# Kernel optimization log

Measured on AMD Instinct MI355X. Metric: run time of the kernel, lower is better.

The kernel has to match this reference:

```python
import jax, jax.numpy as jnp
import numpy as np

NHID = 1024
NHEAD = 16
HEAD_DIM = 64
B, L = 8, 4096

def setup_inputs() -> dict:
    key = jax.random.key(0)
    ks = jax.random.split(key, 12)
    s_in = 1.0 / np.sqrt(NHID)
    s_o = 1.0 / np.sqrt(NHEAD * HEAD_DIM)
    return {
        'x': jax.random.normal(ks[0], (B, L, NHID), dtype=jnp.float32),
        'ax': jax.random.normal(ks[1], (B, NHID), dtype=jnp.float32),
        'WQ_w': jax.random.normal(ks[2], (NHID, NHEAD * HEAD_DIM), dtype=jnp.float32) * s_in,
        'WQ_b': jnp.zeros((NHEAD * HEAD_DIM,), dtype=jnp.float32),
        'WK_w': jax.random.normal(ks[3], (NHID, NHEAD * HEAD_DIM), dtype=jnp.float32) * s_in,
        'WK_b': jnp.zeros((NHEAD * HEAD_DIM,), dtype=jnp.float32),
        'WV_w': jax.random.normal(ks[4], (NHID, NHEAD * HEAD_DIM), dtype=jnp.float32) * s_in,
        'WV_b': jnp.zeros((NHEAD * HEAD_DIM,), dtype=jnp.float32),
        'WO_w': jax.random.normal(ks[5], (NHEAD * HEAD_DIM, NHID), dtype=jnp.float32) * s_o,
        'WO_b': jnp.zeros((NHID,), dtype=jnp.float32),
    }

def reference(x, ax, WQ_w, WQ_b, WK_w, WK_b, WV_w, WV_b, WO_w, WO_b):
    Bx, Lx, H = x.shape
    nh, d = NHEAD, HEAD_DIM
    q = (x @ WQ_w + WQ_b).reshape(Bx, Lx, nh, d)
    k = (x @ WK_w + WK_b).reshape(Bx, Lx, nh, d)
    # global token projections (note: source's v local slots use K due to pad_v=F.pad(k,...) bug)
    ak = (ax @ WK_w + WK_b).reshape(Bx, 1, nh, d)
    av = (ax @ WV_w + WV_b).reshape(Bx, 1, nh, d)
    # shifted local window (unfold_size=3), pad seq dim by 1 on each side
    pad_k = jnp.pad(k, ((0, 0), (1, 1), (0, 0), (0, 0)))  # (B, L+2, nh, d)
    k_shift = jnp.stack([pad_k[:, t:Lx + t] for t in range(3)], axis=3)  # (B,L,nh,3,d)
    akb = jnp.broadcast_to(ak, (Bx, Lx, nh, d))[:, :, :, None, :]  # (B,L,nh,1,d)
    avb = jnp.broadcast_to(av, (Bx, Lx, nh, d))[:, :, :, None, :]
    K = jnp.concatenate([akb, k_shift], axis=3)  # (B,L,nh,4,d)
    V = jnp.concatenate([avb, k_shift], axis=3)  # local V slots = K (faithful to source bug)
    scores = jnp.einsum('blhd,blhjd->blhj', q, K) / jnp.sqrt(jnp.float32(d))
    alphas = jax.nn.softmax(scores, axis=-1)  # dropout = identity (eval)
    att = jnp.einsum('blhj,blhjd->blhd', alphas, V).reshape(Bx, Lx, nh * d)
    return att @ WO_w + WO_b
```

## Files before the change

### kernel.cpp

```cpp
#include <hip/hip_runtime.h>
#include <hip/hip_bf16.h>

typedef __bf16 bf16x8 __attribute__((ext_vector_type(8)));
typedef __bf16 bf16x4 __attribute__((ext_vector_type(4)));
typedef float  floatx4 __attribute__((ext_vector_type(4)));

#define L_SEQ 4096

__global__ void cvt_bf16_kernel(const float* __restrict__ src,
                                __bf16* __restrict__ dst, int n8)
{
    int i = blockIdx.x * blockDim.x + threadIdx.x;
    if (i >= n8) return;
    const float4* s = (const float4*)src + (size_t)i * 2;
    float4 f0 = s[0], f1 = s[1];
    bf16x8 o;
    o[0] = (__bf16)f0.x; o[1] = (__bf16)f0.y; o[2] = (__bf16)f0.z; o[3] = (__bf16)f0.w;
    o[4] = (__bf16)f1.x; o[5] = (__bf16)f1.y; o[6] = (__bf16)f1.z; o[7] = (__bf16)f1.w;
    *((bf16x8*)dst + i) = o;
}

__global__ void transpose_cvt_kernel(const float* __restrict__ src,
                                     __bf16* __restrict__ dst, int K, int N)
{
    __shared__ float tile[32][33];
    int tx = threadIdx.x & 31, ty = threadIdx.x >> 5;
    int n0 = blockIdx.x * 32, k0 = blockIdx.y * 32;
    #pragma unroll
    for (int i = 0; i < 32; i += 8)
        tile[ty + i][tx] = src[(size_t)(k0 + ty + i) * N + n0 + tx];
    __syncthreads();
    #pragma unroll
    for (int i = 0; i < 32; i += 8)
        dst[(size_t)(n0 + ty + i) * K + k0 + tx] = (__bf16)tile[tx][ty + i];
}

__global__ void akv_kernel(const float* __restrict__ ax,
                           const float* __restrict__ Wk, const float* __restrict__ bk,
                           const float* __restrict__ Wv, const float* __restrict__ bv,
                           float* __restrict__ akv)
{
    int b = blockIdx.x, nb = blockIdx.y, kv = blockIdx.z;
    int n = nb * 256 + threadIdx.x;
    const float* W    = kv ? Wv : Wk;
    const float* bias = kv ? bv : bk;
    const float* axr  = ax + (size_t)b * 1024;
    float acc = bias[n];
    for (int k = 0; k < 1024; ++k)
        acc = fmaf(axr[k], W[(size_t)k * 1024 + n], acc);
    akv[((size_t)b * 2 + kv) * 1024 + n] = acc;
}

template <bool OUT_F32>
__global__ __launch_bounds__(256, 2) void gemm_bt_kernel(
    const __bf16* __restrict__ A, const __bf16* __restrict__ Bt,
    const float* __restrict__ b0, const float* __restrict__ b1, int nsplit,
    void* __restrict__ Cp, int M, int N, int K)
{
    __shared__ __bf16 As[128 * 32];
    __shared__ __bf16 Bs[128 * 32];
    const int tid  = threadIdx.x;
    const int wave = tid >> 6, lane = tid & 63;
    const int quad = lane >> 4, l16 = lane & 15;
    const int m0 = blockIdx.x * 128, n0 = blockIdx.y * 128;
    const int wm = (wave >> 1) * 64, wn = (wave & 1) * 64;

    floatx4 acc[4][4] = {};

    const int srow  = lane >> 2;
    const int skcol = (lane & 3) * 8;

    for (int k0 = 0; k0 < K; k0 += 32) {
        if (k0) __syncthreads();
        #pragma unroll
        for (int c = 0; c < 2; ++c) {
            int chunk = wave * 2 + c;
            int row   = chunk * 16 + srow;
            __builtin_amdgcn_global_load_lds(
                (const __attribute__((address_space(1))) void*)(A + (size_t)(m0 + row) * K + k0 + skcol),
                (__attribute__((address_space(3))) void*)(As + chunk * 512),
                16, 0, 0);
            __builtin_amdgcn_global_load_lds(
                (const __attribute__((address_space(1))) void*)(Bt + (size_t)(n0 + row) * K + k0 + skcol),
                (__attribute__((address_space(3))) void*)(Bs + chunk * 512),
                16, 0, 0);
        }
        __syncthreads();

        bf16x8 af[4], bfr[4];
        #pragma unroll
        for (int mi = 0; mi < 4; ++mi)
            af[mi] = *(const bf16x8*)(As + (wm + mi * 16 + l16) * 32 + quad * 8);
        #pragma unroll
        for (int ni = 0; ni < 4; ++ni)
            bfr[ni] = *(const bf16x8*)(Bs + (wn + ni * 16 + l16) * 32 + quad * 8);
        #pragma unroll
        for (int mi = 0; mi < 4; ++mi)
            #pragma unroll
            for (int ni = 0; ni < 4; ++ni)
                acc[mi][ni] = __builtin_amdgcn_mfma_f32_16x16x32_bf16(
                    af[mi], bfr[ni], acc[mi][ni], 0, 0, 0);
    }

    #pragma unroll
    for (int ni = 0; ni < 4; ++ni) {
        int gn = n0 + wn + ni * 16 + l16;
        float bv = (gn < nsplit) ? b0[gn] : b1[gn - nsplit];
        #pragma unroll
        for (int mi = 0; mi < 4; ++mi) {
            int gm = m0 + wm + mi * 16 + quad * 4;
            #pragma unroll
            for (int r = 0; r < 4; ++r) {
                float v = acc[mi][ni][r] + bv;
                if (OUT_F32)
                    ((float*)Cp)[(size_t)(gm + r) * N + gn] = v;
                else
                    ((__bf16*)Cp)[(size_t)(gm + r) * N + gn] = (__bf16)v;
            }
        }
    }
}

__global__ void attn_kernel(const __bf16* __restrict__ qk,
                            const float* __restrict__ akv,
                            __bf16* __restrict__ att)
{
    const int m = blockIdx.x;
    const int l = m & (L_SEQ - 1);
    const int b = m >> 12;
    const int t = threadIdx.x;
    const int c4 = t * 4;

    bf16x4 qv = *(const bf16x4*)(qk + (size_t)m * 2048 + c4);
    float q0 = qv[0], q1 = qv[1], q2 = qv[2], q3 = qv[3];

    float kx[3][4];
    #pragma unroll
    for (int j = 0; j < 3; ++j) {
        int ll = l + j - 1;
        if (ll >= 0 && ll < L_SEQ) {
            bf16x4 kv = *(const bf16x4*)(qk + (size_t)(m + j - 1) * 2048 + 1024 + c4);
            kx[j][0] = kv[0]; kx[j][1] = kv[1]; kx[j][2] = kv[2]; kx[j][3] = kv[3];
        } else {
            kx[j][0] = kx[j][1] = kx[j][2] = kx[j][3] = 0.f;
        }
    }
    const float* akp = akv + ((size_t)b * 2 + 0) * 1024 + c4;
    const float* avp = akv + ((size_t)b * 2 + 1) * 1024 + c4;
    float a0 = akp[0], a1 = akp[1], a2 = akp[2], a3 = akp[3];
    float v0 = avp[0], v1 = avp[1], v2 = avp[2], v3 = avp[3];

    float p0 = q0 * a0 + q1 * a1 + q2 * a2 + q3 * a3;
    float p1 = q0 * kx[0][0] + q1 * kx[0][1] + q2 * kx[0][2] + q3 * kx[0][3];
    float p2 = q0 * kx[1][0] + q1 * kx[1][1] + q2 * kx[1][2] + q3 * kx[1][3];
    float p3 = q0 * kx[2][0] + q1 * kx[2][1] + q2 * kx[2][2] + q3 * kx[2][3];
    #pragma unroll
    for (int off = 1; off < 16; off <<= 1) {
        p0 += __shfl_xor(p0, off, 64);
        p1 += __shfl_xor(p1, off, 64);
        p2 += __shfl_xor(p2, off, 64);
        p3 += __shfl_xor(p3, off, 64);
    }
    const float sc = 0.125f;
    float s0 = p0 * sc, s1 = p1 * sc, s2 = p2 * sc, s3 = p3 * sc;
    float mx = fmaxf(fmaxf(s0, s1), fmaxf(s2, s3));
    float e0 = __expf(s0 - mx), e1 = __expf(s1 - mx), e2 = __expf(s2 - mx), e3 = __expf(s3 - mx);
    float inv = 1.f / (e0 + e1 + e2 + e3);

    bf16x4 o;
    o[0] = (__bf16)((e0 * v0 + e1 * kx[0][0] + e2 * kx[1][0] + e3 * kx[2][0]) * inv);
    o[1] = (__bf16)((e0 * v1 + e1 * kx[0][1] + e2 * kx[1][1] + e3 * kx[2][1]) * inv);
    o[2] = (__bf16)((e0 * v2 + e1 * kx[0][2] + e2 * kx[1][2] + e3 * kx[2][2]) * inv);
    o[3] = (__bf16)((e0 * v3 + e1 * kx[0][3] + e2 * kx[1][3] + e3 * kx[2][3]) * inv);
    *(bf16x4*)(att + (size_t)m * 1024 + c4) = o;
}

extern "C" void kernel_launch(void* const* d_in, const int* in_sizes, int n_in,
                              void* d_out, int out_size, void* d_ws, size_t ws_size,
                              hipStream_t stream)
{
    const float* x    = (const float*)d_in[0];
    const float* ax   = (const float*)d_in[1];
    const float* WQ_w = (const float*)d_in[2];
    const float* WQ_b = (const float*)d_in[3];
    const float* WK_w = (const float*)d_in[4];
    const float* WK_b = (const float*)d_in[5];
    const float* WV_w = (const float*)d_in[6];
    const float* WV_b = (const float*)d_in[7];
    const float* WO_w = (const float*)d_in[8];
    const float* WO_b = (const float*)d_in[9];
    float* out = (float*)d_out;

    const int M = 8 * 4096;

    char* ws = (char*)d_ws;
    __bf16* xb   = (__bf16*)(ws);
    __bf16* Wqk  = (__bf16*)(ws + 67108864);
    __bf16* Wo   = (__bf16*)(ws + 71303168);
    __bf16* qk   = (__bf16*)(ws + 73400320);
    __bf16* att  = (__bf16*)(ws + 207618048);
    float*  akv  = (float*)(ws + 274726912);

    {
        int n8 = (M * 1024) / 8;
        cvt_bf16_kernel<<<n8 / 256, 256, 0, stream>>>(x, xb, n8);
    }
    transpose_cvt_kernel<<<dim3(32, 32), 256, 0, stream>>>(WQ_w, Wqk, 1024, 1024);
    transpose_cvt_kernel<<<dim3(32, 32), 256, 0, stream>>>(WK_w, Wqk + (size_t)1024 * 1024, 1024, 1024);
    transpose_cvt_kernel<<<dim3(32, 32), 256, 0, stream>>>(WO_w, Wo, 1024, 1024);
    akv_kernel<<<dim3(8, 4, 2), 256, 0, stream>>>(ax, WK_w, WK_b, WV_w, WV_b, akv);
    gemm_bt_kernel<false><<<dim3(M / 128, 2048 / 128), 256, 0, stream>>>(
        xb, Wqk, WQ_b, WK_b, 1024, (void*)qk, M, 2048, 1024);
    attn_kernel<<<M, 256, 0, stream>>>(qk, akv, att);
    gemm_bt_kernel<true><<<dim3(M / 128, 1024 / 128), 256, 0, stream>>>(
        att, Wo, WO_b, WO_b, 1024, (void*)out, M, 1024, 1024);
}
```

Before: 632.3 us.

## Remap GEMM tiles per XCD, merge weight transposes, vectorize akv and attention loads

GEMM blocks are launched on a 1D grid and remapped so each XCD (bid&7) owns a fixed set of N tiles, which keeps B-operand tiles resident in that XCD's L2. Launch bounds go from 2 to 4 blocks per SM for more occupancy. The three weight transpose launches become one launch with blockIdx.z choosing the matrix. The akv kernel uses float4 per thread with fewer blocks, and the attention kernel loads akv as float4. The 4-blocks occupancy hint may push register use down and cause spills in the 64-accumulator GEMM.

New measurement: 636.4 us. Within noise of the previous version (+0.6%).

```diff
diff --git a/kernel.cpp b/kernel.cpp
--- a/kernel.cpp
+++ b/kernel.cpp
@@ -20,19 +20,26 @@
     *((bf16x8*)dst + i) = o;
 }
 
-__global__ void transpose_cvt_kernel(const float* __restrict__ src,
-                                     __bf16* __restrict__ dst, int K, int N)
-{
+__global__ void transpose_cvt3_kernel(const float* __restrict__ WQ,
+                                      const float* __restrict__ WK,
+                                      const float* __restrict__ WO,
+                                      __bf16* __restrict__ Wqk,
+                                      __bf16* __restrict__ Wo)
+{
+    const int z = blockIdx.z;
+    const float* src = (z == 0) ? WQ : (z == 1) ? WK : WO;
+    __bf16* dst = (z == 0) ? Wqk : (z == 1) ? (Wqk + (size_t)1024 * 1024) : Wo;
+
     __shared__ float tile[32][33];
     int tx = threadIdx.x & 31, ty = threadIdx.x >> 5;
     int n0 = blockIdx.x * 32, k0 = blockIdx.y * 32;
     #pragma unroll
     for (int i = 0; i < 32; i += 8)
-        tile[ty + i][tx] = src[(size_t)(k0 + ty + i) * N + n0 + tx];
+        tile[ty + i][tx] = src[(size_t)(k0 + ty + i) * 1024 + n0 + tx];
     __syncthreads();
     #pragma unroll
     for (int i = 0; i < 32; i += 8)
-        dst[(size_t)(n0 + ty + i) * K + k0 + tx] = (__bf16)tile[tx][ty + i];
+        dst[(size_t)(n0 + ty + i) * 1024 + k0 + tx] = (__bf16)tile[tx][ty + i];
 }
 
 __global__ void akv_kernel(const float* __restrict__ ax,
@@ -40,29 +47,40 @@
                            const float* __restrict__ Wv, const float* __restrict__ bv,
                            float* __restrict__ akv)
 {
-    int b = blockIdx.x, nb = blockIdx.y, kv = blockIdx.z;
-    int n = nb * 256 + threadIdx.x;
+    int b = blockIdx.x, kv = blockIdx.y;
+    int n = threadIdx.x * 4;
     const float* W    = kv ? Wv : Wk;
     const float* bias = kv ? bv : bk;
     const float* axr  = ax + (size_t)b * 1024;
-    float acc = bias[n];
-    for (int k = 0; k < 1024; ++k)
-        acc = fmaf(axr[k], W[(size_t)k * 1024 + n], acc);
-    akv[((size_t)b * 2 + kv) * 1024 + n] = acc;
-}
-
-template <bool OUT_F32>
-__global__ __launch_bounds__(256, 2) void gemm_bt_kernel(
+    float4 acc = *(const float4*)(bias + n);
+    for (int k = 0; k < 1024; ++k) {
+        float a = axr[k];
+        float4 w = *(const float4*)(W + (size_t)k * 1024 + n);
+        acc.x = fmaf(a, w.x, acc.x);
+        acc.y = fmaf(a, w.y, acc.y);
+        acc.z = fmaf(a, w.z, acc.z);
+        acc.w = fmaf(a, w.w, acc.w);
+    }
+    *(float4*)(akv + ((size_t)b * 2 + kv) * 1024 + n) = acc;
+}
+
+template <int NPX, bool OUT_F32>
+__global__ __launch_bounds__(256, 4) void gemm_bt_kernel(
     const __bf16* __restrict__ A, const __bf16* __restrict__ Bt,
     const float* __restrict__ b0, const float* __restrict__ b1, int nsplit,
     void* __restrict__ Cp, int M, int N, int K)
 {
     __shared__ __bf16 As[128 * 32];
     __shared__ __bf16 Bs[128 * 32];
+    const int bid  = blockIdx.x;
+    const int xcd  = bid & 7, g = bid >> 3;
+    const int nt   = xcd * NPX + (g % NPX);
+    const int mt   = g / NPX;
+    const int m0 = mt * 128, n0 = nt * 128;
+
     const int tid  = threadIdx.x;
     const int wave = tid >> 6, lane = tid & 63;
     const int quad = lane >> 4, l16 = lane & 15;
-    const int m0 = blockIdx.x * 128, n0 = blockIdx.y * 128;
     const int wm = (wave >> 1) * 64, wn = (wave & 1) * 64;
 
     floatx4 acc[4][4] = {};
@@ -145,12 +163,10 @@
             kx[j][0] = kx[j][1] = kx[j][2] = kx[j][3] = 0.f;
         }
     }
-    const float* akp = akv + ((size_t)b * 2 + 0) * 1024 + c4;
-    const float* avp = akv + ((size_t)b * 2 + 1) * 1024 + c4;
-    float a0 = akp[0], a1 = akp[1], a2 = akp[2], a3 = akp[3];
-    float v0 = avp[0], v1 = avp[1], v2 = avp[2], v3 = avp[3];
-
-    float p0 = q0 * a0 + q1 * a1 + q2 * a2 + q3 * a3;
+    float4 av4 = *(const float4*)(akv + ((size_t)b * 2 + 0) * 1024 + c4);
+    float4 vv4 = *(const float4*)(akv + ((size_t)b * 2 + 1) * 1024 + c4);
+
+    float p0 = q0 * av4.x + q1 * av4.y + q2 * av4.z + q3 * av4.w;
     float p1 = q0 * kx[0][0] + q1 * kx[0][1] + q2 * kx[0][2] + q3 * kx[0][3];
     float p2 = q0 * kx[1][0] + q1 * kx[1][1] + q2 * kx[1][2] + q3 * kx[1][3];
     float p3 = q0 * kx[2][0] + q1 * kx[2][1] + q2 * kx[2][2] + q3 * kx[2][3];
@@ -168,10 +184,10 @@
     float inv = 1.f / (e0 + e1 + e2 + e3);
 
     bf16x4 o;
-    o[0] = (__bf16)((e0 * v0 + e1 * kx[0][0] + e2 * kx[1][0] + e3 * kx[2][0]) * inv);
-    o[1] = (__bf16)((e0 * v1 + e1 * kx[0][1] + e2 * kx[1][1] + e3 * kx[2][1]) * inv);
-    o[2] = (__bf16)((e0 * v2 + e1 * kx[0][2] + e2 * kx[1][2] + e3 * kx[2][2]) * inv);
-    o[3] = (__bf16)((e0 * v3 + e1 * kx[0][3] + e2 * kx[1][3] + e3 * kx[2][3]) * inv);
+    o[0] = (__bf16)((e0 * vv4.x + e1 * kx[0][0] + e2 * kx[1][0] + e3 * kx[2][0]) * inv);
+    o[1] = (__bf16)((e0 * vv4.y + e1 * kx[0][1] + e2 * kx[1][1] + e3 * kx[2][1]) * inv);
+    o[2] = (__bf16)((e0 * vv4.z + e1 * kx[0][2] + e2 * kx[1][2] + e3 * kx[2][2]) * inv);
+    o[3] = (__bf16)((e0 * vv4.w + e1 * kx[0][3] + e2 * kx[1][3] + e3 * kx[2][3]) * inv);
     *(bf16x4*)(att + (size_t)m * 1024 + c4) = o;
 }
 
@@ -205,13 +221,11 @@
         int n8 = (M * 1024) / 8;
         cvt_bf16_kernel<<<n8 / 256, 256, 0, stream>>>(x, xb, n8);
     }
-    transpose_cvt_kernel<<<dim3(32, 32), 256, 0, stream>>>(WQ_w, Wqk, 1024, 1024);
-    transpose_cvt_kernel<<<dim3(32, 32), 256, 0, stream>>>(WK_w, Wqk + (size_t)1024 * 1024, 1024, 1024);
-    transpose_cvt_kernel<<<dim3(32, 32), 256, 0, stream>>>(WO_w, Wo, 1024, 1024);
-    akv_kernel<<<dim3(8, 4, 2), 256, 0, stream>>>(ax, WK_w, WK_b, WV_w, WV_b, akv);
-    gemm_bt_kernel<false><<<dim3(M / 128, 2048 / 128), 256, 0, stream>>>(
+    transpose_cvt3_kernel<<<dim3(32, 32, 3), 256, 0, stream>>>(WQ_w, WK_w, WO_w, Wqk, Wo);
+    akv_kernel<<<dim3(8, 2), 256, 0, stream>>>(ax, WK_w, WK_b, WV_w, WV_b, akv);
+    gemm_bt_kernel<2, false><<<(M / 128) * 16, 256, 0, stream>>>(
         xb, Wqk, WQ_b, WK_b, 1024, (void*)qk, M, 2048, 1024);
     attn_kernel<<<M, 256, 0, stream>>>(qk, akv, att);
-    gemm_bt_kernel<true><<<dim3(M / 128, 1024 / 128), 256, 0, stream>>>(
+    gemm_bt_kernel<1, true><<<(M / 128) * 8, 256, 0, stream>>>(
         att, Wo, WO_b, WO_b, 1024, (void*)out, M, 1024, 1024);
 }
```
